# Kernel tuning notes

Measured on AMD Instinct MI355X. Metric: run time of the kernel, lower is better.

## Reference

```python
import jax, jax.numpy as jnp
import numpy as np

D_MODEL = 1024
HIDDEN = 4096
N_EXPERTS = 8
LB_COEF = 0.01
B, N = 2, 2048


def setup_inputs() -> dict:
    key = jax.random.key(0)
    k_x, k_g, k_w1, k_w2 = jax.random.split(key, 4)
    s = 0.02
    return {
        "x": jax.random.normal(k_x, (B, N, D_MODEL), dtype=jnp.float32),
        "gate_w": jax.random.normal(k_g, (N_EXPERTS, D_MODEL), dtype=jnp.float32) * s,
        "w1": jax.random.normal(k_w1, (N_EXPERTS, HIDDEN, D_MODEL), dtype=jnp.float32) * s,  # torch Linear weight [out,in]
        "b1": jnp.zeros((N_EXPERTS, HIDDEN), dtype=jnp.float32),
        "w2": jax.random.normal(k_w2, (N_EXPERTS, D_MODEL, HIDDEN), dtype=jnp.float32) * s,
        "b2": jnp.zeros((N_EXPERTS, D_MODEL), dtype=jnp.float32),
    }


def reference(x, gate_w, w1, b1, w2, b2):
    # gate logits: Linear(d_model, E, bias=False)
    logits = jnp.einsum('bnd,ed->bne', x, gate_w)
    probs = jax.nn.softmax(logits, axis=-1)            # router_prob
    gate_scores = jnp.max(probs, axis=-1)              # top-1 prob [B,N]
    sel = jnp.argmax(probs, axis=-1)                   # selected expert [B,N]

    # load-balance aux loss
    onehot = jax.nn.one_hot(sel, N_EXPERTS, dtype=x.dtype)
    f = onehot.mean(axis=(0, 1))                       # fraction of tokens per expert
    P = probs.mean(axis=(0, 1))                        # mean router prob per expert
    aux_loss = LB_COEF * N_EXPERTS * jnp.sum(f * P)

    # dispatch: loop over fixed small expert count (structurally distinct weights)
    out = jnp.zeros_like(x)
    for e in range(N_EXPERTS):
        h = jax.nn.gelu(jnp.einsum('bnd,hd->bnh', x, w1[e]) + b1[e], approximate=False)
        y = jnp.einsum('bnh,dh->bnd', h, w2[e]) + b2[e]
        out = out + jnp.where((sel == e)[..., None], gate_scores[..., None] * y, jnp.zeros((), x.dtype))
    return out, aux_loss
```

## Files before the change

### kernel.cpp

```cpp
#include <hip/hip_runtime.h>
#include <math.h>

#define T_TOK 4096
#define DM 1024
#define HID 4096
#define NEXP 8
#define MAXT 39
#define NG1  1248

typedef unsigned short u16;
typedef __attribute__((ext_vector_type(8))) short short8;
typedef __attribute__((ext_vector_type(4))) float f32x4;

__device__ __forceinline__ u16 f2bf(float f){
  unsigned u = __float_as_uint(f);
  u += 0x7FFF + ((u >> 16) & 1);
  return (u16)(u >> 16);
}

#define GATE_OFF   0u
#define CNT_OFF    16384u
#define LIST_OFF   16512u
#define PROBS_OFF  147584u
#define XB_OFF     278656u
#define H_OFF      8667264u
#define PART_OFF   42221696u
#define W2B_OFF    109330560u

__device__ __forceinline__ void glds16(const void* g, void* l){
  __builtin_amdgcn_global_load_lds((const __attribute__((address_space(1))) void*)g,
                                   (__attribute__((address_space(3))) void*)l, 16, 0, 0);
}

__global__ void zero_cnt_kernel(int* cnt){
  if (threadIdx.x < NEXP) cnt[threadIdx.x] = 0;
}

__global__ __launch_bounds__(256) void gate_kernel(
    const float* __restrict__ x, const float* __restrict__ gw,
    float* __restrict__ gateo, int* __restrict__ cnt, int* __restrict__ list,
    float* __restrict__ probs, u16* __restrict__ xb)
{
  int tid = threadIdx.x;
  int lane = tid & 63;
  int w = tid >> 6;
  int t = blockIdx.x * 4 + w;

  const float4* x4 = (const float4*)(x + (size_t)t * DM);
  const float4* g4 = (const float4*)gw;

  float acc[8] = {0,0,0,0,0,0,0,0};
  #pragma unroll
  for (int i = 0; i < 4; i++){
    int p = i * 64 + lane;
    float4 xv = x4[p];
    ushort4 pk;
    pk.x = f2bf(xv.x); pk.y = f2bf(xv.y); pk.z = f2bf(xv.z); pk.w = f2bf(xv.w);
    *(ushort4*)&xb[(size_t)t * DM + (size_t)p * 4] = pk;
    #pragma unroll
    for (int e = 0; e < NEXP; e++){
      float4 gv = g4[e * 256 + p];
      acc[e] += xv.x * gv.x + xv.y * gv.y + xv.z * gv.z + xv.w * gv.w;
    }
  }
  #pragma unroll
  for (int e = 0; e < NEXP; e++){
    #pragma unroll
    for (int off = 32; off; off >>= 1)
      acc[e] += __shfl_xor(acc[e], off);
  }
  if (lane == 0){
    float mx = acc[0];
    #pragma unroll
    for (int e = 1; e < NEXP; e++) mx = fmaxf(mx, acc[e]);
    float p[8]; float s = 0.f;
    #pragma unroll
    for (int e = 0; e < NEXP; e++){ p[e] = expf(acc[e] - mx); s += p[e]; }
    float inv = 1.f / s;
    int be = 0; float bp = p[0];
    #pragma unroll
    for (int e = 1; e < NEXP; e++){ if (p[e] > bp){ bp = p[e]; be = e; } }
    #pragma unroll
    for (int e = 0; e < NEXP; e++) probs[(size_t)t * 8 + e] = p[e] * inv;
    gateo[t] = bp * inv;
    int pos = atomicAdd(&cnt[be], 1);
    list[be * T_TOK + pos] = t;
  }
}

__global__ __launch_bounds__(256) void aux_kernel(
    const float* __restrict__ probs, const int* __restrict__ cnt,
    float* __restrict__ aux_out)
{
  __shared__ float sm[256 * 8];
  int tid = threadIdx.x;
  float s[8] = {0,0,0,0,0,0,0,0};
  for (int i = 0; i < 16; i++){
    int t = i * 256 + tid;
    #pragma unroll
    for (int e = 0; e < 8; e++) s[e] += probs[(size_t)t * 8 + e];
  }
  #pragma unroll
  for (int e = 0; e < 8; e++) sm[tid * 8 + e] = s[e];
  __syncthreads();
  for (int st = 128; st; st >>= 1){
    if (tid < st){
      #pragma unroll
      for (int e = 0; e < 8; e++) sm[tid * 8 + e] += sm[(tid + st) * 8 + e];
    }
    __syncthreads();
  }
  if (tid == 0){
    float a = 0.f;
    #pragma unroll
    for (int e = 0; e < 8; e++){
      float f = (float)cnt[e] / (float)T_TOK;
      float P = sm[e] / (float)T_TOK;
      a += f * P;
    }
    aux_out[0] = 0.01f * (float)NEXP * a;
  }
}

__global__ __launch_bounds__(256, 3) void ffn_gemm1(
    const u16*  __restrict__ Aall,
    const float* __restrict__ Bf,
    const float* __restrict__ bias,
    const int*  __restrict__ cnt,
    const int*  __restrict__ list,
    u16*  __restrict__ hOut,
    const float* __restrict__ w2,
    u16*  __restrict__ w2b)
{
  int bid = blockIdx.x;
  int tid = threadIdx.x;

  if (bid >= NG1){
    const size_t TOT = (size_t)NEXP * DM * HID / 8;
    size_t stride = (size_t)512 * 256;
    for (size_t g = (size_t)(bid - NG1) * 256 + tid; g < TOT; g += stride){
      const float4* s = (const float4*)w2 + g * 2;
      float4 a = s[0], c = s[1];
      uint4 p;
      p.x = (unsigned)f2bf(a.x) | ((unsigned)f2bf(a.y) << 16);
      p.y = (unsigned)f2bf(a.z) | ((unsigned)f2bf(a.w) << 16);
      p.z = (unsigned)f2bf(c.x) | ((unsigned)f2bf(c.y) << 16);
      p.w = (unsigned)f2bf(c.z) | ((unsigned)f2bf(c.w) << 16);
      ((uint4*)w2b)[g] = p;
    }
    return;
  }

  constexpr int NT = 32, KS = 16;
  int nt = bid % NT;
  int t  = bid / NT;

  int e = -1, mt = 0, accT = 0;
  #pragma unroll
  for (int i = 0; i < NEXP; i++){
    int nti = (cnt[i] + 127) >> 7;
    if (e < 0 && t < accT + nti){ e = i; mt = t - accT; }
    accT += nti;
  }
  if (e < 0) return;
  int ne = cnt[e];
  int m0 = mt * 128;
  const int* lst = list + e * T_TOK;
  int n0 = nt * 128;

  __shared__ u16 As[8192];
  __shared__ u16 Bs[8192];

  int lane = tid & 63;
  int w    = tid >> 6;
  int wm = w >> 1, wn = w & 1;
  int fr = lane & 15, fq = lane >> 4;

  const u16* aS[4]; int aDst[4];
  #pragma unroll
  for (int i = 0; i < 4; i++){
    int seg = w * 4 + i;
    int rr  = seg * 8 + (lane >> 3);
    int gg  = (lane & 7) ^ (rr & 7);
    int mrow = m0 + rr; if (mrow > ne - 1) mrow = ne - 1;
    aS[i] = Aall + (size_t)lst[mrow] * DM + gg * 8;
    aDst[i] = seg * 512;
  }

  const float* bS[4]; int bDst[4];
  #pragma unroll
  for (int i = 0; i < 4; i++){
    int cc = i * 256 + tid;
    int rr = cc >> 3, sl = cc & 7;
    int gg = sl ^ (rr & 7);
    bS[i] = Bf + ((size_t)e * HID + n0 + rr) * DM + gg * 8;
    bDst[i] = rr * 64 + sl * 8;
  }

  f32x4 acc[4][4];
  #pragma unroll
  for (int m = 0; m < 4; m++)
    #pragma unroll
    for (int n = 0; n < 4; n++)
      acc[m][n] = (f32x4){0.f, 0.f, 0.f, 0.f};

  float4 br0[4], br1[4];
  #pragma unroll
  for (int i = 0; i < 4; i++){
    const float4* s = (const float4*)bS[i];
    br0[i] = s[0]; br1[i] = s[1];
  }

  for (int ks = 0; ks < KS; ++ks){
    if (ks) __syncthreads();
    size_t ko = (size_t)ks * 64;
    #pragma unroll
    for (int i = 0; i < 4; i++) glds16(aS[i] + ko, &As[aDst[i]]);
    #pragma unroll
    for (int i = 0; i < 4; i++){
      uint4 pk;
      pk.x = (unsigned)f2bf(br0[i].x) | ((unsigned)f2bf(br0[i].y) << 16);
      pk.y = (unsigned)f2bf(br0[i].z) | ((unsigned)f2bf(br0[i].w) << 16);
      pk.z = (unsigned)f2bf(br1[i].x) | ((unsigned)f2bf(br1[i].y) << 16);
      pk.w = (unsigned)f2bf(br1[i].z) | ((unsigned)f2bf(br1[i].w) << 16);
      *(uint4*)&Bs[bDst[i]] = pk;
    }
    if (ks + 1 < KS){
      #pragma unroll
      for (int i = 0; i < 4; i++){
        const float4* s = (const float4*)(bS[i] + (ks + 1) * 64);
        br0[i] = s[0]; br1[i] = s[1];
      }
    }
    __syncthreads();
    #pragma unroll
    for (int kc = 0; kc < 2; kc++){
      short8 afr[4], bfr[4];
      #pragma unroll
      for (int m = 0; m < 4; m++){
        int row  = wm * 64 + m * 16 + fr;
        int slot = (kc * 4 + fq) ^ (row & 7);
        afr[m] = *(const short8*)&As[row * 64 + slot * 8];
      }
      #pragma unroll
      for (int n = 0; n < 4; n++){
        int row  = wn * 64 + n * 16 + fr;
        int slot = (kc * 4 + fq) ^ (row & 7);
        bfr[n] = *(const short8*)&Bs[row * 64 + slot * 8];
      }
      #pragma unroll
      for (int m = 0; m < 4; m++)
        #pragma unroll
        for (int n = 0; n < 4; n++)
          acc[m][n] = __builtin_amdgcn_mfma_f32_16x16x32_bf16(afr[m], bfr[n], acc[m][n], 0, 0, 0);
    }
  }

  #pragma unroll
  for (int n = 0; n < 4; n++){
    int col = n0 + wn * 64 + n * 16 + fr;
    float bv = bias[(size_t)e * HID + col];
    #pragma unroll
    for (int m = 0; m < 4; m++){
      int rbase = m0 + wm * 64 + m * 16 + fq * 4;
      f32x4 v = acc[m][n];
      #pragma unroll
      for (int i = 0; i < 4; i++){
        int mrow = rbase + i;
        if (mrow < ne){
          int tok = lst[mrow];
          float val = v[i] + bv;
          float gl = 0.5f * val * (1.0f + erff(val * 0.70710678118654752f));
          hOut[(size_t)tok * HID + col] = f2bf(gl);
        }
      }
    }
  }
}

__global__ __launch_bounds__(256, 3) void ffn_gemm2(
    const u16*  __restrict__ Aall,
    const u16*  __restrict__ Bb,
    const float* __restrict__ bias,
    const int*  __restrict__ cnt,
    const int*  __restrict__ list,
    float* __restrict__ pOut)
{
  constexpr int NT = 8, KS = 16;
  int bid = blockIdx.x;
  int nt = bid % NT;
  int r1 = bid / NT;
  int t  = r1 % MAXT;
  int sk = r1 / MAXT;

  int e = -1, mt = 0, accT = 0;
  #pragma unroll
  for (int i = 0; i < NEXP; i++){
    int nti = (cnt[i] + 127) >> 7;
    if (e < 0 && t < accT + nti){ e = i; mt = t - accT; }
    accT += nti;
  }
  if (e < 0) return;
  int ne = cnt[e];
  int m0 = mt * 128;
  const int* lst = list + e * T_TOK;
  int n0 = nt * 128;
  int koff = sk * (KS * 64);

  __shared__ u16 As[8192];
  __shared__ u16 Bs[8192];

  int tid  = threadIdx.x;
  int lane = tid & 63;
  int w    = tid >> 6;
  int wm = w >> 1, wn = w & 1;
  int fr = lane & 15, fq = lane >> 4;

  const u16* aS[4]; const u16* bS[4]; int dst[4];
  #pragma unroll
  for (int i = 0; i < 4; i++){
    int seg = w * 4 + i;
    int r   = seg * 8 + (lane >> 3);
    int g   = (lane & 7) ^ (r & 7);
    int mrow = m0 + r; if (mrow > ne - 1) mrow = ne - 1;
    aS[i] = Aall + (size_t)lst[mrow] * HID + koff + g * 8;
    bS[i] = Bb + (size_t)e * DM * HID + (size_t)(n0 + r) * HID + koff + g * 8;
    dst[i] = seg * 512;
  }

  f32x4 acc[4][4];
  #pragma unroll
  for (int m = 0; m < 4; m++)
    #pragma unroll
    for (int n = 0; n < 4; n++)
      acc[m][n] = (f32x4){0.f, 0.f, 0.f, 0.f};

  for (int ks = 0; ks < KS; ++ks){
    if (ks) __syncthreads();
    size_t ko = (size_t)ks * 64;
    #pragma unroll
    for (int i = 0; i < 4; i++) glds16(aS[i] + ko, &As[dst[i]]);
    #pragma unroll
    for (int i = 0; i < 4; i++) glds16(bS[i] + ko, &Bs[dst[i]]);
    __syncthreads();
    #pragma unroll
    for (int kc = 0; kc < 2; kc++){
      short8 afr[4], bfr[4];
      #pragma unroll
      for (int m = 0; m < 4; m++){
        int row  = wm * 64 + m * 16 + fr;
        int slot = (kc * 4 + fq) ^ (row & 7);
        afr[m] = *(const short8*)&As[row * 64 + slot * 8];
      }
      #pragma unroll
      for (int n = 0; n < 4; n++){
        int row  = wn * 64 + n * 16 + fr;
        int slot = (kc * 4 + fq) ^ (row & 7);
        bfr[n] = *(const short8*)&Bs[row * 64 + slot * 8];
      }
      #pragma unroll
      for (int m = 0; m < 4; m++)
        #pragma unroll
        for (int n = 0; n < 4; n++)
          acc[m][n] = __builtin_amdgcn_mfma_f32_16x16x32_bf16(afr[m], bfr[n], acc[m][n], 0, 0, 0);
    }
  }

  #pragma unroll
  for (int n = 0; n < 4; n++){
    int col = n0 + wn * 64 + n * 16 + fr;
    float bv = (sk == 0) ? bias[(size_t)e * DM + col] : 0.f;
    #pragma unroll
    for (int m = 0; m < 4; m++){
      int rbase = m0 + wm * 64 + m * 16 + fq * 4;
      f32x4 v = acc[m][n];
      #pragma unroll
      for (int i = 0; i < 4; i++){
        int mrow = rbase + i;
        if (mrow < ne){
          int tok = lst[mrow];
          pOut[((size_t)sk * T_TOK + tok) * DM + col] = v[i] + bv;
        }
      }
    }
  }
}

__global__ __launch_bounds__(256) void reduce_kernel(
    const float* __restrict__ part, const float* __restrict__ gate,
    float* __restrict__ out)
{
  size_t i = (size_t)blockIdx.x * 256 + threadIdx.x;
  constexpr size_t S = (size_t)T_TOK * DM / 4;
  const float4* p = (const float4*)part;
  float4 a = p[i], b = p[i + S], c = p[i + 2 * S], d = p[i + 3 * S];
  float g = gate[i >> 8];
  float4 o;
  o.x = (a.x + b.x + c.x + d.x) * g;
  o.y = (a.y + b.y + c.y + d.y) * g;
  o.z = (a.z + b.z + c.z + d.z) * g;
  o.w = (a.w + b.w + c.w + d.w) * g;
  ((float4*)out)[i] = o;
}

extern "C" void kernel_launch(void* const* d_in, const int* in_sizes, int n_in,
                              void* d_out, int out_size, void* d_ws, size_t ws_size,
                              hipStream_t stream) {
  const float* x   = (const float*)d_in[0];
  const float* gw  = (const float*)d_in[1];
  const float* w1  = (const float*)d_in[2];
  const float* b1  = (const float*)d_in[3];
  const float* w2  = (const float*)d_in[4];
  const float* b2  = (const float*)d_in[5];

  char* ws = (char*)d_ws;
  float* gateo = (float*)(ws + GATE_OFF);
  int*   cnt   = (int*)  (ws + CNT_OFF);
  int*   list  = (int*)  (ws + LIST_OFF);
  float* probs = (float*)(ws + PROBS_OFF);
  u16*   xb    = (u16*)  (ws + XB_OFF);
  u16*   h     = (u16*)  (ws + H_OFF);
  float* part  = (float*)(ws + PART_OFF);
  u16*   w2b   = (u16*)  (ws + W2B_OFF);

  float* out = (float*)d_out;
  float* aux = out + (size_t)T_TOK * DM;

  hipLaunchKernelGGL(zero_cnt_kernel, dim3(1), dim3(64), 0, stream, cnt);
  hipLaunchKernelGGL(gate_kernel, dim3(T_TOK / 4), dim3(256), 0, stream,
                     x, gw, gateo, cnt, list, probs, xb);
  hipLaunchKernelGGL(aux_kernel, dim3(1), dim3(256), 0, stream, probs, cnt, aux);

  hipLaunchKernelGGL(ffn_gemm1, dim3(NG1 + 512), dim3(256), 0, stream,
                     xb, w1, b1, cnt, list, h, w2, w2b);
  hipLaunchKernelGGL(ffn_gemm2, dim3(4 * MAXT * 8), dim3(256), 0, stream,
                     h, w2b, b2, cnt, list, part);
  hipLaunchKernelGGL(reduce_kernel, dim3(T_TOK * DM / 4 / 256), dim3(256), 0, stream,
                     part, gateo, out);
}
```

Before: 296.2 us.

## Pre-convert w1 to bf16 in gate kernel and DMA it directly in GEMM1

Adds 512 extra blocks to the gate kernel that convert all of w1 from fp32 to bf16 into a workspace buffer that aliases the partials region. GEMM1 then loads B tiles with global_load_lds directly into shared memory, the same way it loads A, instead of loading fp32 into registers and packing in the loop. This takes per-tile conversion and register pressure out of GEMM1 and avoids re-reading fp32 w1 across many m-tiles. In exchange it adds a full fp32 read plus a bf16 write of w1 each call, and relies on GEMM2's partials not overwriting w1b before GEMM1 has finished.

```diff
diff --git a/kernel.cpp b/kernel.cpp
--- a/kernel.cpp
+++ b/kernel.cpp
@@ -24,7 +24,8 @@
 #define PROBS_OFF  147584u
 #define XB_OFF     278656u
 #define H_OFF      8667264u
-#define PART_OFF   42221696u
+#define W1B_OFF    42221696u
+#define PART_OFF   W1B_OFF
 #define W2B_OFF    109330560u
 
 __device__ __forceinline__ void glds16(const void* g, void* l){
@@ -39,9 +40,26 @@
 __global__ __launch_bounds__(256) void gate_kernel(
     const float* __restrict__ x, const float* __restrict__ gw,
     float* __restrict__ gateo, int* __restrict__ cnt, int* __restrict__ list,
-    float* __restrict__ probs, u16* __restrict__ xb)
+    float* __restrict__ probs, u16* __restrict__ xb,
+    const float* __restrict__ w1, u16* __restrict__ w1b)
 {
   int tid = threadIdx.x;
+  if (blockIdx.x >= 1024){
+    const size_t TOT = (size_t)NEXP * HID * DM / 8;
+    size_t stride = (size_t)512 * 256;
+    for (size_t g = (size_t)(blockIdx.x - 1024) * 256 + tid; g < TOT; g += stride){
+      const float4* s = (const float4*)w1 + g * 2;
+      float4 a = s[0], c = s[1];
+      uint4 p;
+      p.x = (unsigned)f2bf(a.x) | ((unsigned)f2bf(a.y) << 16);
+      p.y = (unsigned)f2bf(a.z) | ((unsigned)f2bf(a.w) << 16);
+      p.z = (unsigned)f2bf(c.x) | ((unsigned)f2bf(c.y) << 16);
+      p.w = (unsigned)f2bf(c.z) | ((unsigned)f2bf(c.w) << 16);
+      ((uint4*)w1b)[g] = p;
+    }
+    return;
+  }
+
   int lane = tid & 63;
   int w = tid >> 6;
   int t = blockIdx.x * 4 + w;
@@ -124,7 +142,7 @@
 
 __global__ __launch_bounds__(256, 3) void ffn_gemm1(
     const u16*  __restrict__ Aall,
-    const float* __restrict__ Bf,
+    const u16*  __restrict__ Bb,
     const float* __restrict__ bias,
     const int*  __restrict__ cnt,
     const int*  __restrict__ list,
@@ -176,25 +194,16 @@
   int wm = w >> 1, wn = w & 1;
   int fr = lane & 15, fq = lane >> 4;
 
-  const u16* aS[4]; int aDst[4];
+  const u16* aS[4]; const u16* bS[4]; int dst[4];
   #pragma unroll
   for (int i = 0; i < 4; i++){
     int seg = w * 4 + i;
-    int rr  = seg * 8 + (lane >> 3);
-    int gg  = (lane & 7) ^ (rr & 7);
-    int mrow = m0 + rr; if (mrow > ne - 1) mrow = ne - 1;
-    aS[i] = Aall + (size_t)lst[mrow] * DM + gg * 8;
-    aDst[i] = seg * 512;
-  }
-
-  const float* bS[4]; int bDst[4];
-  #pragma unroll
-  for (int i = 0; i < 4; i++){
-    int cc = i * 256 + tid;
-    int rr = cc >> 3, sl = cc & 7;
-    int gg = sl ^ (rr & 7);
-    bS[i] = Bf + ((size_t)e * HID + n0 + rr) * DM + gg * 8;
-    bDst[i] = rr * 64 + sl * 8;
+    int r   = seg * 8 + (lane >> 3);
+    int g   = (lane & 7) ^ (r & 7);
+    int mrow = m0 + r; if (mrow > ne - 1) mrow = ne - 1;
+    aS[i] = Aall + (size_t)lst[mrow] * DM + g * 8;
+    bS[i] = Bb + (size_t)e * HID * DM + (size_t)(n0 + r) * DM + g * 8;
+    dst[i] = seg * 512;
   }
 
   f32x4 acc[4][4];
@@ -203,35 +212,14 @@
     #pragma unroll
     for (int n = 0; n < 4; n++)
       acc[m][n] = (f32x4){0.f, 0.f, 0.f, 0.f};
-
-  float4 br0[4], br1[4];
-  #pragma unroll
-  for (int i = 0; i < 4; i++){
-    const float4* s = (const float4*)bS[i];
-    br0[i] = s[0]; br1[i] = s[1];
-  }
 
   for (int ks = 0; ks < KS; ++ks){
     if (ks) __syncthreads();
     size_t ko = (size_t)ks * 64;
     #pragma unroll
-    for (int i = 0; i < 4; i++) glds16(aS[i] + ko, &As[aDst[i]]);
-    #pragma unroll
-    for (int i = 0; i < 4; i++){
-      uint4 pk;
-      pk.x = (unsigned)f2bf(br0[i].x) | ((unsigned)f2bf(br0[i].y) << 16);
-      pk.y = (unsigned)f2bf(br0[i].z) | ((unsigned)f2bf(br0[i].w) << 16);
-      pk.z = (unsigned)f2bf(br1[i].x) | ((unsigned)f2bf(br1[i].y) << 16);
-      pk.w = (unsigned)f2bf(br1[i].z) | ((unsigned)f2bf(br1[i].w) << 16);
-      *(uint4*)&Bs[bDst[i]] = pk;
-    }
-    if (ks + 1 < KS){
-      #pragma unroll
-      for (int i = 0; i < 4; i++){
-        const float4* s = (const float4*)(bS[i] + (ks + 1) * 64);
-        br0[i] = s[0]; br1[i] = s[1];
-      }
-    }
+    for (int i = 0; i < 4; i++) glds16(aS[i] + ko, &As[dst[i]]);
+    #pragma unroll
+    for (int i = 0; i < 4; i++) glds16(bS[i] + ko, &Bs[dst[i]]);
     __syncthreads();
     #pragma unroll
     for (int kc = 0; kc < 2; kc++){
@@ -420,6 +408,7 @@
   float* probs = (float*)(ws + PROBS_OFF);
   u16*   xb    = (u16*)  (ws + XB_OFF);
   u16*   h     = (u16*)  (ws + H_OFF);
+  u16*   w1b   = (u16*)  (ws + W1B_OFF);
   float* part  = (float*)(ws + PART_OFF);
   u16*   w2b   = (u16*)  (ws + W2B_OFF);
 
@@ -427,12 +416,12 @@
   float* aux = out + (size_t)T_TOK * DM;
 
   hipLaunchKernelGGL(zero_cnt_kernel, dim3(1), dim3(64), 0, stream, cnt);
-  hipLaunchKernelGGL(gate_kernel, dim3(T_TOK / 4), dim3(256), 0, stream,
-                     x, gw, gateo, cnt, list, probs, xb);
+  hipLaunchKernelGGL(gate_kernel, dim3(1536), dim3(256), 0, stream,
+                     x, gw, gateo, cnt, list, probs, xb, w1, w1b);
   hipLaunchKernelGGL(aux_kernel, dim3(1), dim3(256), 0, stream, probs, cnt, aux);
 
   hipLaunchKernelGGL(ffn_gemm1, dim3(NG1 + 512), dim3(256), 0, stream,
-                     xb, w1, b1, cnt, list, h, w2, w2b);
+                     xb, w1b, b1, cnt, list, h, w2, w2b);
   hipLaunchKernelGGL(ffn_gemm2, dim3(4 * MAXT * 8), dim3(256), 0, stream,
                      h, w2b, b2, cnt, list, part);
   hipLaunchKernelGGL(reduce_kernel, dim3(T_TOK * DM / 4 / 256), dim3(256), 0, stream,
```

After: 300.9 us. About the same (+1.6%).

## Fuse split-K reduction into GEMM2 via atomics and fold aux loss into GEMM1

Applied to the files above, without the earlier changes.

GEMM2 now scales its split-K partial results by the gate score and atomically adds them straight into the zeroed output. This removes the 64 MB partial buffer write, the reduce kernel's read of it and one launch. The aux-loss reduction moves into an extra block of the GEMM1 launch, which drops another launch. In exchange it adds a memset of the output, float atomics contending across the 4 K-splits, and a summation order that is no longer deterministic.

```diff
diff --git a/kernel.cpp b/kernel.cpp
--- a/kernel.cpp
+++ b/kernel.cpp
@@ -24,7 +24,6 @@
 #define PROBS_OFF  147584u
 #define XB_OFF     278656u
 #define H_OFF      8667264u
-#define PART_OFF   42221696u
 #define W2B_OFF    109330560u
 
 __device__ __forceinline__ void glds16(const void* g, void* l){
@@ -88,40 +87,6 @@
   }
 }
 
-__global__ __launch_bounds__(256) void aux_kernel(
-    const float* __restrict__ probs, const int* __restrict__ cnt,
-    float* __restrict__ aux_out)
-{
-  __shared__ float sm[256 * 8];
-  int tid = threadIdx.x;
-  float s[8] = {0,0,0,0,0,0,0,0};
-  for (int i = 0; i < 16; i++){
-    int t = i * 256 + tid;
-    #pragma unroll
-    for (int e = 0; e < 8; e++) s[e] += probs[(size_t)t * 8 + e];
-  }
-  #pragma unroll
-  for (int e = 0; e < 8; e++) sm[tid * 8 + e] = s[e];
-  __syncthreads();
-  for (int st = 128; st; st >>= 1){
-    if (tid < st){
-      #pragma unroll
-      for (int e = 0; e < 8; e++) sm[tid * 8 + e] += sm[(tid + st) * 8 + e];
-    }
-    __syncthreads();
-  }
-  if (tid == 0){
-    float a = 0.f;
-    #pragma unroll
-    for (int e = 0; e < 8; e++){
-      float f = (float)cnt[e] / (float)T_TOK;
-      float P = sm[e] / (float)T_TOK;
-      a += f * P;
-    }
-    aux_out[0] = 0.01f * (float)NEXP * a;
-  }
-}
-
 __global__ __launch_bounds__(256, 3) void ffn_gemm1(
     const u16*  __restrict__ Aall,
     const float* __restrict__ Bf,
@@ -130,10 +95,46 @@
     const int*  __restrict__ list,
     u16*  __restrict__ hOut,
     const float* __restrict__ w2,
-    u16*  __restrict__ w2b)
+    u16*  __restrict__ w2b,
+    const float* __restrict__ probs,
+    float* __restrict__ aux_out)
 {
   int bid = blockIdx.x;
   int tid = threadIdx.x;
+
+  __shared__ u16 As[8192];
+  __shared__ u16 Bs[8192];
+
+  if (bid == NG1 + 512){
+    float* sm = (float*)As;
+    float s[8] = {0,0,0,0,0,0,0,0};
+    for (int i = 0; i < 16; i++){
+      int t = i * 256 + tid;
+      #pragma unroll
+      for (int e = 0; e < 8; e++) s[e] += probs[(size_t)t * 8 + e];
+    }
+    #pragma unroll
+    for (int e = 0; e < 8; e++) sm[tid * 8 + e] = s[e];
+    __syncthreads();
+    for (int st = 128; st; st >>= 1){
+      if (tid < st){
+        #pragma unroll
+        for (int e = 0; e < 8; e++) sm[tid * 8 + e] += sm[(tid + st) * 8 + e];
+      }
+      __syncthreads();
+    }
+    if (tid == 0){
+      float a = 0.f;
+      #pragma unroll
+      for (int e = 0; e < 8; e++){
+        float f = (float)cnt[e] / (float)T_TOK;
+        float P = sm[e] / (float)T_TOK;
+        a += f * P;
+      }
+      aux_out[0] = 0.01f * (float)NEXP * a;
+    }
+    return;
+  }
 
   if (bid >= NG1){
     const size_t TOT = (size_t)NEXP * DM * HID / 8;
@@ -168,9 +169,6 @@
   const int* lst = list + e * T_TOK;
   int n0 = nt * 128;
 
-  __shared__ u16 As[8192];
-  __shared__ u16 Bs[8192];
-
   int lane = tid & 63;
   int w    = tid >> 6;
   int wm = w >> 1, wn = w & 1;
@@ -284,7 +282,8 @@
     const float* __restrict__ bias,
     const int*  __restrict__ cnt,
     const int*  __restrict__ list,
-    float* __restrict__ pOut)
+    const float* __restrict__ gate,
+    float* __restrict__ out)
 {
   constexpr int NT = 8, KS = 16;
   int bid = blockIdx.x;
@@ -379,28 +378,11 @@
         int mrow = rbase + i;
         if (mrow < ne){
           int tok = lst[mrow];
-          pOut[((size_t)sk * T_TOK + tok) * DM + col] = v[i] + bv;
+          atomicAdd(&out[(size_t)tok * DM + col], gate[tok] * (v[i] + bv));
         }
       }
     }
   }
-}
-
-__global__ __launch_bounds__(256) void reduce_kernel(
-    const float* __restrict__ part, const float* __restrict__ gate,
-    float* __restrict__ out)
-{
-  size_t i = (size_t)blockIdx.x * 256 + threadIdx.x;
-  constexpr size_t S = (size_t)T_TOK * DM / 4;
-  const float4* p = (const float4*)part;
-  float4 a = p[i], b = p[i + S], c = p[i + 2 * S], d = p[i + 3 * S];
-  float g = gate[i >> 8];
-  float4 o;
-  o.x = (a.x + b.x + c.x + d.x) * g;
-  o.y = (a.y + b.y + c.y + d.y) * g;
-  o.z = (a.z + b.z + c.z + d.z) * g;
-  o.w = (a.w + b.w + c.w + d.w) * g;
-  ((float4*)out)[i] = o;
 }
 
 extern "C" void kernel_launch(void* const* d_in, const int* in_sizes, int n_in,
@@ -420,21 +402,18 @@
   float* probs = (float*)(ws + PROBS_OFF);
   u16*   xb    = (u16*)  (ws + XB_OFF);
   u16*   h     = (u16*)  (ws + H_OFF);
-  float* part  = (float*)(ws + PART_OFF);
   u16*   w2b   = (u16*)  (ws + W2B_OFF);
 
   float* out = (float*)d_out;
   float* aux = out + (size_t)T_TOK * DM;
 
+  hipMemsetAsync(d_out, 0, (size_t)out_size * sizeof(float), stream);
   hipLaunchKernelGGL(zero_cnt_kernel, dim3(1), dim3(64), 0, stream, cnt);
   hipLaunchKernelGGL(gate_kernel, dim3(T_TOK / 4), dim3(256), 0, stream,
                      x, gw, gateo, cnt, list, probs, xb);
-  hipLaunchKernelGGL(aux_kernel, dim3(1), dim3(256), 0, stream, probs, cnt, aux);
-
-  hipLaunchKernelGGL(ffn_gemm1, dim3(NG1 + 512), dim3(256), 0, stream,
-                     xb, w1, b1, cnt, list, h, w2, w2b);
+
+  hipLaunchKernelGGL(ffn_gemm1, dim3(NG1 + 512 + 1), dim3(256), 0, stream,
+                     xb, w1, b1, cnt, list, h, w2, w2b, probs, aux);
   hipLaunchKernelGGL(ffn_gemm2, dim3(4 * MAXT * 8), dim3(256), 0, stream,
-                     h, w2b, b2, cnt, list, part);
-  hipLaunchKernelGGL(reduce_kernel, dim3(T_TOK * DM / 4 / 256), dim3(256), 0, stream,
-                     part, gateo, out);
-}
+                     h, w2b, b2, cnt, list, gateo, out);
+}
```

Result: slower. 356.1 us (+20.2%).
